# Optimization experiments

Measured on AMD Instinct MI355X. Metric: run time of the kernel, lower is better.

The kernel has to match this reference:

```python
import jax, jax.numpy as jnp
import numpy as np


def _mlp3(x, w0, b0, w1, b1, w2, b2):
    x = jax.nn.relu(x @ w0.T + b0)
    x = jax.nn.relu(x @ w1.T + b1)
    return x @ w2.T + b2


def setup_inputs() -> dict:
    key = jax.random.key(0)
    ks = jax.random.split(key, 32)
    B, T, C, E, H, A = 64, 256, 53, 64, 64, 128
    C2 = C * C
    s = 0.1  # weight scale for numerical stability
    inp = {
        'x': jax.random.normal(ks[0], (B, T, C), jnp.float32),
        'w_emb': s * jax.random.normal(ks[1], (E, 1), jnp.float32),
        'b_emb': s * jax.random.normal(ks[2], (E,), jnp.float32),
        'w_ih': s * jax.random.normal(ks[3], (3 * H, E), jnp.float32),
        'w_hh': s * jax.random.normal(ks[4], (3 * H, H), jnp.float32),
        'b_ih': s * jax.random.normal(ks[5], (3 * H,), jnp.float32),
        'b_hh': s * jax.random.normal(ks[6], (3 * H,), jnp.float32),
        'q_w0': s * jax.random.normal(ks[7], (A, H), jnp.float32),
        'q_b0': s * jax.random.normal(ks[8], (A,), jnp.float32),
        'q_w1': s * jax.random.normal(ks[9], (A, A), jnp.float32),
        'q_b1': s * jax.random.normal(ks[10], (A,), jnp.float32),
        'q_w2': s * jax.random.normal(ks[11], (A, A), jnp.float32),
        'q_b2': s * jax.random.normal(ks[12], (A,), jnp.float32),
        'k_w0': s * jax.random.normal(ks[13], (A, H), jnp.float32),
        'k_b0': s * jax.random.normal(ks[14], (A,), jnp.float32),
        'k_w1': s * jax.random.normal(ks[15], (A, A), jnp.float32),
        'k_b1': s * jax.random.normal(ks[16], (A,), jnp.float32),
        'k_w2': s * jax.random.normal(ks[17], (A, A), jnp.float32),
        'k_b2': s * jax.random.normal(ks[18], (A,), jnp.float32),
        'gate_bias': jax.random.normal(ks[19], (C, C), jnp.float32),
        'pred_w': s * jax.random.normal(ks[20], (1, H), jnp.float32),
        'pred_b': s * jax.random.normal(ks[21], (1,), jnp.float32),
        'clf_w0': 0.02 * jax.random.normal(ks[22], (C2 // 2, C2), jnp.float32),
        'clf_b0': s * jax.random.normal(ks[23], (C2 // 2,), jnp.float32),
        'clf_w1': 0.02 * jax.random.normal(ks[24], (C2 // 4, C2 // 2), jnp.float32),
        'clf_b1': s * jax.random.normal(ks[25], (C2 // 4,), jnp.float32),
        'clf_w2': 0.02 * jax.random.normal(ks[26], (2, C2 // 4), jnp.float32),
        'clf_b2': s * jax.random.normal(ks[27], (2,), jnp.float32),
    }
    return inp


def reference(x, w_emb, b_emb, w_ih, w_hh, b_ih, b_hh,
              q_w0, q_b0, q_w1, q_b1, q_w2, q_b2,
              k_w0, k_b0, k_w1, k_b1, k_w2, k_b2,
              gate_bias, pred_w, pred_b,
              clf_w0, clf_b0, clf_w1, clf_b1, clf_w2, clf_b2):
    B, T, C = x.shape
    H = w_hh.shape[1]
    # single_embed Linear(1, E): embedded[b,t,c,e] = x[b,t,c]*w[e] + b[e]
    embedded = x[..., None] * w_emb[:, 0] + b_emb          # (B,T,C,E)
    emb_t = jnp.transpose(embedded, (1, 0, 2, 3))           # (T,B,C,E)
    h0 = jnp.zeros((B, C, H), x.dtype)

    def step(h, e_t):
        # GRU cell over B*C independent sequences (vectorized as (B,C,*))
        gi = e_t @ w_ih.T + b_ih                            # (B,C,3H)
        gh = h @ w_hh.T + b_hh
        ir, iz, inn = jnp.split(gi, 3, axis=-1)
        hr, hz, hn = jnp.split(gh, 3, axis=-1)
        r = jax.nn.sigmoid(ir + hr)
        z = jax.nn.sigmoid(iz + hz)
        n = jnp.tanh(inn + r * hn)
        h_gru = (1.0 - z) * n + z * h                       # (B,C,H)
        # gated self-attention mixing across components
        q = _mlp3(h_gru, q_w0, q_b0, q_w1, q_b1, q_w2, q_b2)
        k = _mlp3(h_gru, k_w0, k_b0, k_w1, k_b1, k_w2, k_b2)
        transfer = jnp.einsum('bch,bdh->bcd', q, k)         # (B,C,C)
        norms = jnp.sqrt(jnp.sum(transfer * transfer, axis=(1, 2), keepdims=True))
        transfer = transfer / norms                         # Frobenius matrix-norm divide
        gate = jax.nn.sigmoid(jnp.abs(transfer) + gate_bias)
        transfer = transfer * gate
        h_new = jnp.einsum('bcd,bdh->bch', transfer, h_gru)
        return h_new, (h_new, transfer)

    _, (hs, mix) = jax.lax.scan(step, h0, emb_t)
    hs = jnp.transpose(hs, (1, 0, 2, 3))                    # (B,T,C,H)
    mix = jnp.transpose(mix, (1, 0, 2, 3))                  # (B,T,C,C)

    hidden = hs[:, :-1]                                     # (B,T-1,C,H)
    predicted = (hidden @ pred_w.T + pred_b)[..., 0]        # (B,T-1,C)

    clf_in = mix.reshape(B, T, -1)                          # (B,T,C^2)
    mean_FNC = jnp.mean(clf_in, axis=1).reshape(B, C, C)
    z1 = jax.nn.relu(clf_in @ clf_w0.T + clf_b0)            # dropout is identity (eval)
    z2 = jax.nn.relu(z1 @ clf_w1.T + clf_b1)
    logits = jnp.mean(z2 @ clf_w2.T + clf_b2, axis=1)       # (B,2)
    return (logits, mean_FNC, mix, predicted, x[:, 1:, :])
```

## Files before the change

kernel.cpp:

```cpp
#include <hip/hip_runtime.h>
#include <hip/hip_fp16.h>

typedef _Float16 f16;
typedef f16 f16x4 __attribute__((ext_vector_type(4)));
typedef f16 f16x8 __attribute__((ext_vector_type(8)));
typedef float f32x4 __attribute__((ext_vector_type(4)));
typedef float f32x4u __attribute__((ext_vector_type(4), aligned(4)));

#define DEVINL __device__ __forceinline__
#define MFMA16(a, b, c) __builtin_amdgcn_mfma_f32_16x16x32_f16(a, b, c, 0, 0, 0)

DEVINL float sigmoidf_(float v) { return 1.f / (1.f + __expf(-v)); }


__global__ __launch_bounds__(512)
void scan_kernel(const float* __restrict__ x,
                 const float* __restrict__ w_emb,
                 const float* __restrict__ b_emb,
                 const float* __restrict__ w_ih,
                 const float* __restrict__ w_hh,
                 const float* __restrict__ b_ih,
                 const float* __restrict__ b_hh,
                 const float* __restrict__ qw0, const float* __restrict__ qb0,
                 const float* __restrict__ qw1, const float* __restrict__ qb1,
                 const float* __restrict__ qw2, const float* __restrict__ qb2,
                 const float* __restrict__ kw0, const float* __restrict__ kb0,
                 const float* __restrict__ kw1, const float* __restrict__ kb1,
                 const float* __restrict__ kw2, const float* __restrict__ kb2,
                 const float* __restrict__ gate_bias,
                 const float* __restrict__ pred_w,
                 const float* __restrict__ pred_b,
                 float* __restrict__ out_meanF,
                 float* __restrict__ out_mix,
                 float* __restrict__ out_pred,
                 float* __restrict__ out_xcopy)
{
    extern __shared__ __align__(16) unsigned char smem[];
    float* hh  = (float*)smem;
    f16*   hK  = (f16*)(smem + 15232);
    f16*   hC  = (f16*)(smem + 23424);
    f16*   qk0 = (f16*)(smem + 31616);
    f16*   qk1 = (f16*)(smem + 48000);
    f16*   qk2 = (f16*)(smem + 64384);
    f16*   qk3 = (f16*)(smem + 80768);
    f16*   gh  = (f16*)(smem + 31616);
    f16*   trK = (f16*)(smem + 31616);
    float* xc  = (float*)(smem + 97152);
    float* pw  = (float*)(smem + 97376);
    float* red = (float*)(smem + 97632);

    const int b    = blockIdx.x;
    const int tid  = threadIdx.x;
    const int wv   = tid >> 6;
    const int lane = tid & 63;
    const int quad = lane >> 4;
    const int l15  = lane & 15;
    const int colg = (wv << 3) + (lane >> 3);
    const int rsub = lane & 7;

#define FRAG(buf, kt, nt) ((buf) + ((((kt) * 4 + (nt)) * 64 + lane) * 8))

    for (int i = tid; i < 56 * 68; i += 512) hh[i] = 0.f;
    for (int i = tid; i < 4096; i += 512) { hK[i] = (f16)0.f; hC[i] = (f16)0.f; }
    if (tid < 56) xc[tid] = 0.f;
    if (tid < 64) pw[tid] = pred_w[tid];

    float a_r = 0.f, a_z = 0.f, a_n = 0.f, s_r = 0.f, s_z = 0.f, s_n = 0.f;
    for (int e = 0; e < 64; e++) {
        float we = w_emb[e], be = b_emb[e];
        float w0 = w_ih[colg * 64 + e];
        float w1 = w_ih[(64 + colg) * 64 + e];
        float w2 = w_ih[(128 + colg) * 64 + e];
        a_r += w0 * we; s_r += w0 * be;
        a_z += w1 * we; s_z += w1 * be;
        a_n += w2 * we; s_n += w2 * be;
    }
    const float c_r = s_r + b_ih[colg] + b_hh[colg];
    const float c_z = s_z + b_ih[64 + colg] + b_hh[64 + colg];
    const float c_n = s_n + b_ih[128 + colg];
    const float bhn = b_hh[128 + colg];
    const float pb  = pred_b[0];

    auto ldfrag = [&](const float* W, int K, int mt, int kt) -> f16x8 {
        const float* p = W + (size_t)(mt * 16 + l15) * K + kt * 32 + quad * 8;
        float4 u0 = *(const float4*)p;
        float4 u1 = *(const float4*)(p + 4);
        f16x8 a;
        a[0] = (f16)u0.x; a[1] = (f16)u0.y; a[2] = (f16)u0.z; a[3] = (f16)u0.w;
        a[4] = (f16)u1.x; a[5] = (f16)u1.y; a[6] = (f16)u1.z; a[7] = (f16)u1.w;
        return a;
    };

    const int mtLo = (6 * wv) >> 2, mtHi = (6 * wv + 5) >> 2;
    f16x8 wg0k0 = ldfrag(w_hh, 64, mtLo, 0), wg0k1 = ldfrag(w_hh, 64, mtLo, 1);
    f16x8 wg1k0 = ldfrag(w_hh, 64, mtHi, 0), wg1k1 = ldfrag(w_hh, 64, mtHi, 1);

    f16x8 wq0f[2], wk0f[2], wq1f[4], wq2f[4], wk1f[4], wk2f[4];
#pragma unroll
    for (int kt = 0; kt < 2; kt++) {
        wq0f[kt] = ldfrag(qw0, 64, wv, kt);
        wk0f[kt] = ldfrag(kw0, 64, wv, kt);
    }
#pragma unroll
    for (int kt = 0; kt < 4; kt++) {
        wq1f[kt] = ldfrag(qw1, 128, wv, kt);
        wq2f[kt] = ldfrag(qw2, 128, wv, kt);
        wk1f[kt] = ldfrag(kw1, 128, wv, kt);
        wk2f[kt] = ldfrag(kw2, 128, wv, kt);
    }

    const int f0 = wv * 16 + quad * 4;
    f32x4 bq0v, bq1v, bq2v, bk0v, bk1v, bk2v;
#pragma unroll
    for (int r = 0; r < 4; r++) {
        bq0v[r] = qb0[f0 + r]; bq1v[r] = qb1[f0 + r]; bq2v[r] = qb2[f0 + r];
        bk0v[r] = kb0[f0 + r]; bk1v[r] = kb1[f0 + r]; bk2v[r] = kb2[f0 + r];
    }

    const int tmt = wv & 3, tnt0 = (wv >> 2) * 2;
    float gbv[8], mf[8];
#pragma unroll
    for (int i = 0; i < 2; i++)
#pragma unroll
        for (int r = 0; r < 4; r++) {
            int c = tmt * 16 + quad * 4 + r, d = (tnt0 + i) * 16 + l15;
            gbv[i * 4 + r] = (c < 53 && d < 53) ? gate_bias[c * 53 + d] : 0.f;
            mf[i * 4 + r] = 0.f;
        }

    auto cwrite = [&](f16* dst, int ct, const f32x4 acc, const f32x4 bv, bool rel) {
        const int kts  = wv >> 1;
        const int sub  = (2 * wv + (quad >> 1)) & 3;
        const int base = ((kts * 4 + ct) * 64 + (l15 + 16 * sub)) * 8 + (quad & 1) * 4;
        f16x4 p;
#pragma unroll
        for (int r = 0; r < 4; r++) {
            float v = acc[r] + bv[r];
            if (rel) v = fmaxf(v, 0.f);
            p[r] = (f16)v;
        }
        *(f16x4*)(dst + base) = p;
    };

    __syncthreads();

#define MLP4X(WF, SRC, DST, BV, REL) do { \
    f32x4 a0 = {0.f,0.f,0.f,0.f}, a1 = {0.f,0.f,0.f,0.f}; \
    f32x4 a2 = {0.f,0.f,0.f,0.f}, a3 = {0.f,0.f,0.f,0.f}; \
    _Pragma("unroll") for (int kt = 0; kt < 4; kt++) { \
        a0 = MFMA16(WF[kt], *(const f16x8*)FRAG(SRC, kt, 0), a0); \
        a1 = MFMA16(WF[kt], *(const f16x8*)FRAG(SRC, kt, 1), a1); \
        a2 = MFMA16(WF[kt], *(const f16x8*)FRAG(SRC, kt, 2), a2); \
        a3 = MFMA16(WF[kt], *(const f16x8*)FRAG(SRC, kt, 3), a3); } \
    cwrite(DST, 0, a0, BV, REL); cwrite(DST, 1, a1, BV, REL); \
    cwrite(DST, 2, a2, BV, REL); cwrite(DST, 3, a3, BV, REL); } while (0)

    float xv = 0.f;
    if (tid < 53) xv = x[(size_t)b * 256 * 53 + tid];

    for (int t = 0; t < 256; t++) {
        if (tid < 53) xc[tid] = xv;
        {
#pragma unroll
            for (int i = 0; i < 6; i++) {
                int tau = 6 * wv + i, mt = tau >> 2, ct = tau & 3;
                bool hi = (mt != mtLo);
                f32x4 acc = {0.f, 0.f, 0.f, 0.f};
                acc = MFMA16(hi ? wg1k0 : wg0k0, *(const f16x8*)FRAG(hK, 0, ct), acc);
                acc = MFMA16(hi ? wg1k1 : wg0k1, *(const f16x8*)FRAG(hK, 1, ct), acc);
                int gbase = (mt * 16 + quad * 4) * 68 + ct * 16 + l15;
#pragma unroll
                for (int r = 0; r < 4; r++) gh[gbase + r * 68] = (f16)acc[r];
            }
        }
        __syncthreads();
        {
#pragma unroll
            for (int r = 0; r < 7; r++) {
                int c = rsub + 8 * r;
                float hr = (float)gh[colg * 68 + c];
                float hz = (float)gh[(64 + colg) * 68 + c];
                float hn = (float)gh[(128 + colg) * 68 + c];
                float xcv = xc[c];
                float hp = hh[c * 68 + colg];
                float rr = sigmoidf_(xcv * a_r + c_r + hr);
                float zz = sigmoidf_(xcv * a_z + c_z + hz);
                float e2 = __expf(2.f * (xcv * a_n + c_n + rr * (hn + bhn)));
                float nn = 1.f - 2.f / (e2 + 1.f);
                float hg = (1.f - zz) * nn + zz * hp;
                hh[c * 68 + colg] = hg;
                f16 h6 = (f16)hg;
                hK[(((colg >> 5) * 4 + (c >> 4)) * 64 + (c & 15) + 16 * ((colg >> 3) & 3)) * 8 + (colg & 7)] = h6;
                hC[(((c >> 5) * 4 + (colg >> 4)) * 64 + (colg & 15) + 16 * ((c >> 3) & 3)) * 8 + (c & 7)] = h6;
            }
        }
        __syncthreads();
        {
            if (tid < 53) {
                if (t >= 1) out_xcopy[(b * 255 + (t - 1)) * 53 + tid] = xv;
                if (t < 255) xv = x[((size_t)b * 256 + t + 1) * 53 + tid];
            }
            f32x4 a0 = {0.f,0.f,0.f,0.f}, a1 = {0.f,0.f,0.f,0.f};
            f32x4 a2 = {0.f,0.f,0.f,0.f}, a3 = {0.f,0.f,0.f,0.f};
#pragma unroll
            for (int kt = 0; kt < 2; kt++) {
                a0 = MFMA16(wq0f[kt], *(const f16x8*)FRAG(hK, kt, 0), a0);
                a1 = MFMA16(wq0f[kt], *(const f16x8*)FRAG(hK, kt, 1), a1);
                a2 = MFMA16(wq0f[kt], *(const f16x8*)FRAG(hK, kt, 2), a2);
                a3 = MFMA16(wq0f[kt], *(const f16x8*)FRAG(hK, kt, 3), a3);
            }
            cwrite(qk0, 0, a0, bq0v, true); cwrite(qk0, 1, a1, bq0v, true);
            cwrite(qk0, 2, a2, bq0v, true); cwrite(qk0, 3, a3, bq0v, true);
            f32x4 k0 = {0.f,0.f,0.f,0.f}, k1 = {0.f,0.f,0.f,0.f};
            f32x4 k2 = {0.f,0.f,0.f,0.f}, k3 = {0.f,0.f,0.f,0.f};
#pragma unroll
            for (int kt = 0; kt < 2; kt++) {
                k0 = MFMA16(wk0f[kt], *(const f16x8*)FRAG(hK, kt, 0), k0);
                k1 = MFMA16(wk0f[kt], *(const f16x8*)FRAG(hK, kt, 1), k1);
                k2 = MFMA16(wk0f[kt], *(const f16x8*)FRAG(hK, kt, 2), k2);
                k3 = MFMA16(wk0f[kt], *(const f16x8*)FRAG(hK, kt, 3), k3);
            }
            cwrite(qk1, 0, k0, bk0v, true); cwrite(qk1, 1, k1, bk0v, true);
            cwrite(qk1, 2, k2, bk0v, true); cwrite(qk1, 3, k3, bk0v, true);
        }
        __syncthreads();
        MLP4X(wq1f, qk0, qk2, bq1v, true);
        MLP4X(wk1f, qk1, qk3, bk1v, true);
        __syncthreads();
        MLP4X(wq2f, qk2, qk0, bq2v, false);
        MLP4X(wk2f, qk3, qk1, bk2v, false);
        __syncthreads();
        f32x4 tacc0 = {0.f,0.f,0.f,0.f}, tacc1 = {0.f,0.f,0.f,0.f};
        {
            f16x8 qa[4];
#pragma unroll
            for (int kt = 0; kt < 4; kt++) qa[kt] = *(const f16x8*)FRAG(qk0, kt, tmt);
#pragma unroll
            for (int kt = 0; kt < 4; kt++) {
                tacc0 = MFMA16(qa[kt], *(const f16x8*)FRAG(qk1, kt, tnt0), tacc0);
                tacc1 = MFMA16(qa[kt], *(const f16x8*)FRAG(qk1, kt, tnt0 + 1), tacc1);
            }
            float ssq = 0.f;
#pragma unroll
            for (int r = 0; r < 4; r++) {
                int c = tmt * 16 + quad * 4 + r;
                if (c < 53) {
                    if (tnt0 * 16 + l15 < 53)       ssq += tacc0[r] * tacc0[r];
                    if ((tnt0 + 1) * 16 + l15 < 53) ssq += tacc1[r] * tacc1[r];
                }
            }
#pragma unroll
            for (int off = 32; off > 0; off >>= 1) ssq += __shfl_down(ssq, off);
            if (lane == 0) red[wv] = ssq;
        }
        __syncthreads();
        float ov[8];
        {
            float s2 = 0.f;
#pragma unroll
            for (int w8 = 0; w8 < 8; w8++) s2 += red[w8];
            const float inv = rsqrtf(s2);
#pragma unroll
            for (int i = 0; i < 2; i++)
#pragma unroll
                for (int r = 0; r < 4; r++) {
                    int c = tmt * 16 + quad * 4 + r;
                    int d = (tnt0 + i) * 16 + l15;
                    float v = (i == 0 ? tacc0[r] : tacc1[r]) * inv;
                    float g = sigmoidf_(fabsf(v) + gbv[i * 4 + r]);
                    v *= g;
                    bool ok = (c < 53) & (d < 53);
                    v = ok ? v : 0.f;
                    ov[i * 4 + r] = v;
                    mf[i * 4 + r] += v;
                    trK[(((d >> 5) * 4 + (c >> 4)) * 64 + (c & 15) + 16 * ((d >> 3) & 3)) * 8 + (d & 7)] = (f16)v;
                }
        }
        __syncthreads();
        {
            const int mixbase = (b * 256 + t) * 2809;
#pragma unroll
            for (int i = 0; i < 2; i++)
#pragma unroll
                for (int r = 0; r < 4; r++) {
                    int c = tmt * 16 + quad * 4 + r;
                    int d = (tnt0 + i) * 16 + l15;
                    if ((c < 53) & (d < 53)) out_mix[mixbase + c * 53 + d] = ov[i * 4 + r];
                }
        }
        {
            f32x4 h0 = {0.f,0.f,0.f,0.f}, h1 = {0.f,0.f,0.f,0.f};
            f16x8 ta0 = *(const f16x8*)FRAG(trK, 0, tmt);
            f16x8 ta1 = *(const f16x8*)FRAG(trK, 1, tmt);
            h0 = MFMA16(ta0, *(const f16x8*)FRAG(hC, 0, tnt0), h0);
            h0 = MFMA16(ta1, *(const f16x8*)FRAG(hC, 1, tnt0), h0);
            h1 = MFMA16(ta0, *(const f16x8*)FRAG(hC, 0, tnt0 + 1), h1);
            h1 = MFMA16(ta1, *(const f16x8*)FRAG(hC, 1, tnt0 + 1), h1);
#pragma unroll
            for (int i = 0; i < 2; i++)
#pragma unroll
                for (int r = 0; r < 4; r++) {
                    int c = tmt * 16 + quad * 4 + r;
                    int e = (tnt0 + i) * 16 + l15;
                    float v = (i == 0 ? h0[r] : h1[r]);
                    if (c < 56) hh[c * 68 + e] = v;
                    hK[(((e >> 5) * 4 + (c >> 4)) * 64 + (c & 15) + 16 * ((e >> 3) & 3)) * 8 + (e & 7)] = (f16)v;
                }
        }
        __syncthreads();
        if (t < 255 && tid < 53) {
            const float* hrow = hh + tid * 68;
            float s = pb;
#pragma unroll 4
            for (int e4 = 0; e4 < 16; e4++) {
                float4 hv = *(const float4*)(hrow + e4 * 4);
                float4 wv4 = *(const float4*)(pw + e4 * 4);
                s += hv.x * wv4.x + hv.y * wv4.y + hv.z * wv4.z + hv.w * wv4.w;
            }
            out_pred[(b * 255 + t) * 53 + tid] = s;
        }
    }

#pragma unroll
    for (int i = 0; i < 2; i++)
#pragma unroll
        for (int r = 0; r < 4; r++) {
            int c = tmt * 16 + quad * 4 + r;
            int d = (tnt0 + i) * 16 + l15;
            if (c < 53 && d < 53)
                out_meanF[b * 2809 + c * 53 + d] = mf[i * 4 + r] * (1.f / 256.f);
        }
#undef FRAG
#undef MLP4X
}

DEVINL void cvt16(const float* p, f16x8& lo, f16x8& hi) {
    f32x4u u0 = *(const f32x4u*)p;
    f32x4u u1 = *(const f32x4u*)(p + 4);
    f32x4u u2 = *(const f32x4u*)(p + 8);
    f32x4u u3 = *(const f32x4u*)(p + 12);
    lo[0] = (f16)u0.x; lo[1] = (f16)u0.y; lo[2] = (f16)u0.z; lo[3] = (f16)u0.w;
    lo[4] = (f16)u1.x; lo[5] = (f16)u1.y; lo[6] = (f16)u1.z; lo[7] = (f16)u1.w;
    hi[0] = (f16)u2.x; hi[1] = (f16)u2.y; hi[2] = (f16)u2.z; hi[3] = (f16)u2.w;
    hi[4] = (f16)u3.x; hi[5] = (f16)u3.y; hi[6] = (f16)u3.z; hi[7] = (f16)u3.w;
}

template<bool AHALF, bool COLSUM>
__global__ __launch_bounds__(256)
void clf_mfma(const void* __restrict__ Ap,
              const float* __restrict__ W,
              const float* __restrict__ bias,
              __half* __restrict__ z_out,
              float* __restrict__ colsum_out,
              int N, int K, int lda, int Kpad, int ldz)
{
    __shared__ __align__(16) f16 As[4096];
    __shared__ __align__(16) f16 Bs[4096];

    const int tid  = threadIdx.x;
    const int wv   = tid >> 6;
    const int lane = tid & 63;
    const int quad = lane >> 4;
    const int l15  = lane & 15;
    const int wm   = wv & 1;
    const int wn   = wv >> 1;
    const int m0   = blockIdx.x * 128;
    const int n0   = blockIdx.y * 128;

    const int srow = tid >> 1;
    const int skh  = (tid & 1) * 16;
    const int sdst = ((srow >> 4) * 64 + (skh >> 3) * 16 + (srow & 15)) * 8;

    f32x4 acc[4][4];
#pragma unroll
    for (int i = 0; i < 4; i++)
#pragma unroll
        for (int j = 0; j < 4; j++)
            acc[i][j] = (f32x4){0.f, 0.f, 0.f, 0.f};

    for (int k0 = 0; k0 < Kpad; k0 += 32) {
        {
            f16x8 lo, hi;
            if constexpr (AHALF) {
                const f16* p = (const f16*)Ap + (size_t)(m0 + srow) * lda + k0 + skh;
                lo = *(const f16x8*)p;
                hi = *(const f16x8*)(p + 8);
            } else {
                const float* p = (const float*)Ap + (size_t)(m0 + srow) * lda + k0 + skh;
                if (k0 + 32 <= K) {
                    cvt16(p, lo, hi);
                } else {
                    int kr = K - (k0 + skh);
#pragma unroll
                    for (int j = 0; j < 8; j++) lo[j] = (f16)((j < kr) ? p[j] : 0.f);
#pragma unroll
                    for (int j = 0; j < 8; j++) hi[j] = (f16)((j + 8 < kr) ? p[j + 8] : 0.f);
                }
            }
            *(f16x8*)(As + sdst)       = lo;
            *(f16x8*)(As + sdst + 128) = hi;
        }
        {
            f16x8 lo, hi;
#pragma unroll
            for (int j = 0; j < 8; j++) { lo[j] = (f16)0.f; hi[j] = (f16)0.f; }
            const int nrow = n0 + srow;
            if (nrow < N) {
                const float* p = W + (size_t)nrow * K + k0 + skh;
                if (k0 + 32 <= K) {
                    cvt16(p, lo, hi);
                } else {
                    int kr = K - (k0 + skh);
#pragma unroll
                    for (int j = 0; j < 8; j++) lo[j] = (f16)((j < kr) ? p[j] : 0.f);
#pragma unroll
                    for (int j = 0; j < 8; j++) hi[j] = (f16)((j + 8 < kr) ? p[j + 8] : 0.f);
                }
            }
            *(f16x8*)(Bs + sdst)       = lo;
            *(f16x8*)(Bs + sdst + 128) = hi;
        }
        __syncthreads();
        {
            f16x8 afr[4], bfr[4];
#pragma unroll
            for (int i = 0; i < 4; i++)
                afr[i] = *(const f16x8*)(As + ((wm * 4 + i) * 64 + lane) * 8);
#pragma unroll
            for (int i = 0; i < 4; i++)
                bfr[i] = *(const f16x8*)(Bs + ((wn * 4 + i) * 64 + lane) * 8);
#pragma unroll
            for (int mi = 0; mi < 4; mi++)
#pragma unroll
                for (int ni = 0; ni < 4; ni++)
                    acc[mi][ni] = MFMA16(afr[mi], bfr[ni], acc[mi][ni]);
        }
        __syncthreads();
    }

    if constexpr (!COLSUM) {
#pragma unroll
        for (int ni = 0; ni < 4; ni++) {
            int n = n0 + wn * 64 + ni * 16 + l15;
            float bj = (n < N) ? bias[n] : 0.f;
#pragma unroll
            for (int mi = 0; mi < 4; mi++) {
                int m = m0 + wm * 64 + mi * 16 + quad * 4;
#pragma unroll
                for (int r = 0; r < 4; r++) {
                    float v = (n < N) ? fmaxf(acc[mi][ni][r] + bj, 0.f) : 0.f;
                    z_out[(size_t)(m + r) * ldz + n] = __float2half(v);
                }
            }
        }
    } else {
        const int batch = m0 >> 8;
#pragma unroll
        for (int ni = 0; ni < 4; ni++) {
            int n = n0 + wn * 64 + ni * 16 + l15;
            float bj = (n < N) ? bias[n] : 0.f;
            float s = 0.f;
#pragma unroll
            for (int mi = 0; mi < 4; mi++)
#pragma unroll
                for (int r = 0; r < 4; r++)
                    s += fmaxf(acc[mi][ni][r] + bj, 0.f);
            s += __shfl_down(s, 32);
            s += __shfl_down(s, 16);
            if (quad == 0 && n < N)
                atomicAdd(&colsum_out[batch * 704 + n], s);
        }
    }
}

__global__ __launch_bounds__(128)
void logits_kernel(const float* __restrict__ zsum,
                   const float* __restrict__ w2,
                   const float* __restrict__ b2,
                   float* __restrict__ out)
{
    int tid = threadIdx.x;
    int bb = tid >> 1, o = tid & 1;
    const float* zs = zsum + bb * 704;
    const float* wrow = w2 + o * 702;
    float s = 0.f;
    for (int j = 0; j < 702; j++) s += zs[j] * wrow[j];
    out[bb * 2 + o] = s * (1.f / 256.f) + b2[o];
}

extern "C" void kernel_launch(void* const* d_in, const int* in_sizes, int n_in,
                              void* d_out, int out_size, void* d_ws, size_t ws_size,
                              hipStream_t stream)
{
    const float* x      = (const float*)d_in[0];
    const float* w_emb  = (const float*)d_in[1];
    const float* b_emb  = (const float*)d_in[2];
    const float* w_ih   = (const float*)d_in[3];
    const float* w_hh   = (const float*)d_in[4];
    const float* b_ih   = (const float*)d_in[5];
    const float* b_hh   = (const float*)d_in[6];
    const float* qw0 = (const float*)d_in[7];
    const float* qb0 = (const float*)d_in[8];
    const float* qw1 = (const float*)d_in[9];
    const float* qb1 = (const float*)d_in[10];
    const float* qw2 = (const float*)d_in[11];
    const float* qb2 = (const float*)d_in[12];
    const float* kw0 = (const float*)d_in[13];
    const float* kb0 = (const float*)d_in[14];
    const float* kw1 = (const float*)d_in[15];
    const float* kb1 = (const float*)d_in[16];
    const float* kw2 = (const float*)d_in[17];
    const float* kb2 = (const float*)d_in[18];
    const float* gate_bias = (const float*)d_in[19];
    const float* pred_w = (const float*)d_in[20];
    const float* pred_b = (const float*)d_in[21];
    const float* cw0 = (const float*)d_in[22];
    const float* cb0 = (const float*)d_in[23];
    const float* cw1 = (const float*)d_in[24];
    const float* cb1 = (const float*)d_in[25];
    const float* cw2 = (const float*)d_in[26];
    const float* cb2 = (const float*)d_in[27];

    float* out_logits = (float*)d_out;
    float* out_meanF  = (float*)d_out + 128;
    float* out_mix    = (float*)d_out + 128 + 179776;
    float* out_pred   = out_mix + 46022656;
    float* out_xcopy  = out_pred + 864960;

    float*  zsum = (float*)d_ws;
    __half* z1   = (__half*)((char*)d_ws + (1 << 18));

    static int s_attr_done = 0;
    if (!s_attr_done) {
        hipFuncSetAttribute((const void*)scan_kernel,
                            hipFuncAttributeMaxDynamicSharedMemorySize, 98304);
        s_attr_done = 1;
    }

    hipMemsetAsync(zsum, 0, 64 * 704 * sizeof(float), stream);

    scan_kernel<<<64, 512, 97680, stream>>>(
        x, w_emb, b_emb, w_ih, w_hh, b_ih, b_hh,
        qw0, qb0, qw1, qb1, qw2, qb2,
        kw0, kb0, kw1, kb1, kw2, kb2,
        gate_bias, pred_w, pred_b,
        out_meanF, out_mix, out_pred, out_xcopy);

    clf_mfma<false, false><<<dim3(128, 11), 256, 0, stream>>>(
        out_mix, cw0, cb0, z1, nullptr, 1404, 2809, 2809, 2816, 1408);

    clf_mfma<true, true><<<dim3(128, 6), 256, 0, stream>>>(
        z1, cw1, cb1, nullptr, zsum, 702, 1404, 1408, 1408, 0);

    logits_kernel<<<1, 128, 0, stream>>>(zsum, cw2, cb2, out_logits);
}
```

Before: 3.217 ms.

## Process two batch elements per scan block to interleave independent recurrences

The scan kernel now handles two batch sequences per workgroup (32 blocks instead of 64). Each block keeps duplicated shared-memory state for both and interleaves their MFMA stages between the same barriers. The goal is to amortize barrier and latency cost across two independent dependency chains and hide MFMA latency with more ILP. In exchange it uses half the CUs, roughly doubles per-block work, and needs about 162KB of LDS. That exceeds the 64KB documented LDS per workgroup on CDNA3, and MI355X's larger LDS would have to accommodate it. The x load and copy also move from a one-step prefetch to a synchronous load at each step.

New measurement: 7.797 ms. 2.42x slower.

```diff
diff --git a/kernel.cpp b/kernel.cpp
--- a/kernel.cpp
+++ b/kernel.cpp
@@ -36,20 +36,7 @@
                  float* __restrict__ out_xcopy)
 {
     extern __shared__ __align__(16) unsigned char smem[];
-    float* hh  = (float*)smem;
-    f16*   hK  = (f16*)(smem + 15232);
-    f16*   hC  = (f16*)(smem + 23424);
-    f16*   qk0 = (f16*)(smem + 31616);
-    f16*   qk1 = (f16*)(smem + 48000);
-    f16*   qk2 = (f16*)(smem + 64384);
-    f16*   qk3 = (f16*)(smem + 80768);
-    f16*   gh  = (f16*)(smem + 31616);
-    f16*   trK = (f16*)(smem + 31616);
-    float* xc  = (float*)(smem + 97152);
-    float* pw  = (float*)(smem + 97376);
-    float* red = (float*)(smem + 97632);
-
-    const int b    = blockIdx.x;
+
     const int tid  = threadIdx.x;
     const int wv   = tid >> 6;
     const int lane = tid & 63;
@@ -58,11 +45,33 @@
     const int colg = (wv << 3) + (lane >> 3);
     const int rsub = lane & 7;
 
+    float* hh[2]; f16 *hK[2], *hC[2], *qkX[2], *qkY[2], *qkZ[2], *ghp[2], *trKp[2];
+#pragma unroll
+    for (int p = 0; p < 2; p++) {
+        unsigned char* r = smem + p * 80768;
+        hh[p]  = (float*)r;
+        hK[p]  = (f16*)(r + 15232);
+        hC[p]  = (f16*)(r + 23424);
+        qkX[p] = (f16*)(r + 31616);
+        qkY[p] = (f16*)(r + 48000);
+        qkZ[p] = (f16*)(r + 64384);
+        ghp[p] = (f16*)(r + 31616);
+        trKp[p]= (f16*)(r + 31616);
+    }
+    unsigned char* tail = smem + 161536;
+    float* xc[2]  = {(float*)tail, (float*)(tail + 224)};
+    float* pw     = (float*)(tail + 448);
+    float* red[2] = {(float*)(tail + 704), (float*)(tail + 736)};
+
+    const int bb[2] = {(int)blockIdx.x * 2, (int)blockIdx.x * 2 + 1};
+
 #define FRAG(buf, kt, nt) ((buf) + ((((kt) * 4 + (nt)) * 64 + lane) * 8))
 
-    for (int i = tid; i < 56 * 68; i += 512) hh[i] = 0.f;
-    for (int i = tid; i < 4096; i += 512) { hK[i] = (f16)0.f; hC[i] = (f16)0.f; }
-    if (tid < 56) xc[tid] = 0.f;
+#pragma unroll
+    for (int p = 0; p < 2; p++) {
+        for (int i = tid; i < 56 * 68; i += 512) hh[p][i] = 0.f;
+        for (int i = tid; i < 4096; i += 512) { hK[p][i] = (f16)0.f; hC[p][i] = (f16)0.f; }
+    }
     if (tid < 64) pw[tid] = pred_w[tid];
 
     float a_r = 0.f, a_z = 0.f, a_n = 0.f, s_r = 0.f, s_z = 0.f, s_n = 0.f;
@@ -118,184 +127,189 @@
     }
 
     const int tmt = wv & 3, tnt0 = (wv >> 2) * 2;
-    float gbv[8], mf[8];
+    float gbv[8], mf[2][8];
 #pragma unroll
     for (int i = 0; i < 2; i++)
 #pragma unroll
         for (int r = 0; r < 4; r++) {
             int c = tmt * 16 + quad * 4 + r, d = (tnt0 + i) * 16 + l15;
             gbv[i * 4 + r] = (c < 53 && d < 53) ? gate_bias[c * 53 + d] : 0.f;
-            mf[i * 4 + r] = 0.f;
+            mf[0][i * 4 + r] = 0.f; mf[1][i * 4 + r] = 0.f;
         }
 
     auto cwrite = [&](f16* dst, int ct, const f32x4 acc, const f32x4 bv, bool rel) {
         const int kts  = wv >> 1;
         const int sub  = (2 * wv + (quad >> 1)) & 3;
         const int base = ((kts * 4 + ct) * 64 + (l15 + 16 * sub)) * 8 + (quad & 1) * 4;
-        f16x4 p;
+        f16x4 pk;
 #pragma unroll
         for (int r = 0; r < 4; r++) {
             float v = acc[r] + bv[r];
             if (rel) v = fmaxf(v, 0.f);
-            p[r] = (f16)v;
-        }
-        *(f16x4*)(dst + base) = p;
+            pk[r] = (f16)v;
+        }
+        *(f16x4*)(dst + base) = pk;
     };
 
+    auto mlp4 = [&](const f16x8* WF, const f16* SRC, f16* DST, const f32x4 bv, bool rel) {
+        f32x4 a0 = {0.f,0.f,0.f,0.f}, a1 = {0.f,0.f,0.f,0.f};
+        f32x4 a2 = {0.f,0.f,0.f,0.f}, a3 = {0.f,0.f,0.f,0.f};
+#pragma unroll
+        for (int kt = 0; kt < 4; kt++) {
+            a0 = MFMA16(WF[kt], *(const f16x8*)FRAG(SRC, kt, 0), a0);
+            a1 = MFMA16(WF[kt], *(const f16x8*)FRAG(SRC, kt, 1), a1);
+            a2 = MFMA16(WF[kt], *(const f16x8*)FRAG(SRC, kt, 2), a2);
+            a3 = MFMA16(WF[kt], *(const f16x8*)FRAG(SRC, kt, 3), a3);
+        }
+        cwrite(DST, 0, a0, bv, rel); cwrite(DST, 1, a1, bv, rel);
+        cwrite(DST, 2, a2, bv, rel); cwrite(DST, 3, a3, bv, rel);
+    };
+
     __syncthreads();
 
-#define MLP4X(WF, SRC, DST, BV, REL) do { \
-    f32x4 a0 = {0.f,0.f,0.f,0.f}, a1 = {0.f,0.f,0.f,0.f}; \
-    f32x4 a2 = {0.f,0.f,0.f,0.f}, a3 = {0.f,0.f,0.f,0.f}; \
-    _Pragma("unroll") for (int kt = 0; kt < 4; kt++) { \
-        a0 = MFMA16(WF[kt], *(const f16x8*)FRAG(SRC, kt, 0), a0); \
-        a1 = MFMA16(WF[kt], *(const f16x8*)FRAG(SRC, kt, 1), a1); \
-        a2 = MFMA16(WF[kt], *(const f16x8*)FRAG(SRC, kt, 2), a2); \
-        a3 = MFMA16(WF[kt], *(const f16x8*)FRAG(SRC, kt, 3), a3); } \
-    cwrite(DST, 0, a0, BV, REL); cwrite(DST, 1, a1, BV, REL); \
-    cwrite(DST, 2, a2, BV, REL); cwrite(DST, 3, a3, BV, REL); } while (0)
-
-    float xv = 0.f;
-    if (tid < 53) xv = x[(size_t)b * 256 * 53 + tid];
+    f32x4 tacc0[2], tacc1[2];
 
     for (int t = 0; t < 256; t++) {
-        if (tid < 53) xc[tid] = xv;
-        {
+        if (tid < 53) {
+#pragma unroll
+            for (int p = 0; p < 2; p++) {
+                float xv = x[((size_t)bb[p] * 256 + t) * 53 + tid];
+                xc[p][tid] = xv;
+                if (t >= 1) out_xcopy[((size_t)bb[p] * 255 + (t - 1)) * 53 + tid] = xv;
+            }
+        }
+#pragma unroll
+        for (int p = 0; p < 2; p++) {
 #pragma unroll
             for (int i = 0; i < 6; i++) {
                 int tau = 6 * wv + i, mt = tau >> 2, ct = tau & 3;
                 bool hi = (mt != mtLo);
                 f32x4 acc = {0.f, 0.f, 0.f, 0.f};
-                acc = MFMA16(hi ? wg1k0 : wg0k0, *(const f16x8*)FRAG(hK, 0, ct), acc);
-                acc = MFMA16(hi ? wg1k1 : wg0k1, *(const f16x8*)FRAG(hK, 1, ct), acc);
+                acc = MFMA16(hi ? wg1k0 : wg0k0, *(const f16x8*)FRAG(hK[p], 0, ct), acc);
+                acc = MFMA16(hi ? wg1k1 : wg0k1, *(const f16x8*)FRAG(hK[p], 1, ct), acc);
                 int gbase = (mt * 16 + quad * 4) * 68 + ct * 16 + l15;
 #pragma unroll
-                for (int r = 0; r < 4; r++) gh[gbase + r * 68] = (f16)acc[r];
-            }
-        }
-        __syncthreads();
-        {
+                for (int r = 0; r < 4; r++) ghp[p][gbase + r * 68] = (f16)acc[r];
+            }
+        }
+        __syncthreads();
+#pragma unroll
+        for (int p = 0; p < 2; p++) {
 #pragma unroll
             for (int r = 0; r < 7; r++) {
                 int c = rsub + 8 * r;
-                float hr = (float)gh[colg * 68 + c];
-                float hz = (float)gh[(64 + colg) * 68 + c];
-                float hn = (float)gh[(128 + colg) * 68 + c];
-                float xcv = xc[c];
-                float hp = hh[c * 68 + colg];
+                float hr = (float)ghp[p][colg * 68 + c];
+                float hz = (float)ghp[p][(64 + colg) * 68 + c];
+                float hn = (float)ghp[p][(128 + colg) * 68 + c];
+                float xcv = xc[p][c];
+                float hp = hh[p][c * 68 + colg];
                 float rr = sigmoidf_(xcv * a_r + c_r + hr);
                 float zz = sigmoidf_(xcv * a_z + c_z + hz);
                 float e2 = __expf(2.f * (xcv * a_n + c_n + rr * (hn + bhn)));
                 float nn = 1.f - 2.f / (e2 + 1.f);
                 float hg = (1.f - zz) * nn + zz * hp;
-                hh[c * 68 + colg] = hg;
+                hh[p][c * 68 + colg] = hg;
                 f16 h6 = (f16)hg;
-                hK[(((colg >> 5) * 4 + (c >> 4)) * 64 + (c & 15) + 16 * ((colg >> 3) & 3)) * 8 + (colg & 7)] = h6;
-                hC[(((c >> 5) * 4 + (colg >> 4)) * 64 + (colg & 15) + 16 * ((c >> 3) & 3)) * 8 + (c & 7)] = h6;
-            }
-        }
-        __syncthreads();
-        {
-            if (tid < 53) {
-                if (t >= 1) out_xcopy[(b * 255 + (t - 1)) * 53 + tid] = xv;
-                if (t < 255) xv = x[((size_t)b * 256 + t + 1) * 53 + tid];
-            }
+                hK[p][(((colg >> 5) * 4 + (c >> 4)) * 64 + (c & 15) + 16 * ((colg >> 3) & 3)) * 8 + (colg & 7)] = h6;
+                hC[p][(((c >> 5) * 4 + (colg >> 4)) * 64 + (colg & 15) + 16 * ((c >> 3) & 3)) * 8 + (c & 7)] = h6;
+            }
+        }
+        __syncthreads();
+#pragma unroll
+        for (int p = 0; p < 2; p++) {
             f32x4 a0 = {0.f,0.f,0.f,0.f}, a1 = {0.f,0.f,0.f,0.f};
             f32x4 a2 = {0.f,0.f,0.f,0.f}, a3 = {0.f,0.f,0.f,0.f};
 #pragma unroll
             for (int kt = 0; kt < 2; kt++) {
-                a0 = MFMA16(wq0f[kt], *(const f16x8*)FRAG(hK, kt, 0), a0);
-                a1 = MFMA16(wq0f[kt], *(const f16x8*)FRAG(hK, kt, 1), a1);
-                a2 = MFMA16(wq0f[kt], *(const f16x8*)FRAG(hK, kt, 2), a2);
-                a3 = MFMA16(wq0f[kt], *(const f16x8*)FRAG(hK, kt, 3), a3);
-            }
-            cwrite(qk0, 0, a0, bq0v, true); cwrite(qk0, 1, a1, bq0v, true);
-            cwrite(qk0, 2, a2, bq0v, true); cwrite(qk0, 3, a3, bq0v, true);
+                a0 = MFMA16(wq0f[kt], *(const f16x8*)FRAG(hK[p], kt, 0), a0);
+                a1 = MFMA16(wq0f[kt], *(const f16x8*)FRAG(hK[p], kt, 1), a1);
+                a2 = MFMA16(wq0f[kt], *(const f16x8*)FRAG(hK[p], kt, 2), a2);
+                a3 = MFMA16(wq0f[kt], *(const f16x8*)FRAG(hK[p], kt, 3), a3);
+            }
+            cwrite(qkX[p], 0, a0, bq0v, true); cwrite(qkX[p], 1, a1, bq0v, true);
+            cwrite(qkX[p], 2, a2, bq0v, true); cwrite(qkX[p], 3, a3, bq0v, true);
             f32x4 k0 = {0.f,0.f,0.f,0.f}, k1 = {0.f,0.f,0.f,0.f};
             f32x4 k2 = {0.f,0.f,0.f,0.f}, k3 = {0.f,0.f,0.f,0.f};
 #pragma unroll
             for (int kt = 0; kt < 2; kt++) {
-                k0 = MFMA16(wk0f[kt], *(const f16x8*)FRAG(hK, kt, 0), k0);
-                k1 = MFMA16(wk0f[kt], *(const f16x8*)FRAG(hK, kt, 1), k1);
-                k2 = MFMA16(wk0f[kt], *(const f16x8*)FRAG(hK, kt, 2), k2);
-                k3 = MFMA16(wk0f[kt], *(const f16x8*)FRAG(hK, kt, 3), k3);
-            }
-            cwrite(qk1, 0, k0, bk0v, true); cwrite(qk1, 1, k1, bk0v, true);
-            cwrite(qk1, 2, k2, bk0v, true); cwrite(qk1, 3, k3, bk0v, true);
-        }
-        __syncthreads();
-        MLP4X(wq1f, qk0, qk2, bq1v, true);
-        MLP4X(wk1f, qk1, qk3, bk1v, true);
-        __syncthreads();
-        MLP4X(wq2f, qk2, qk0, bq2v, false);
-        MLP4X(wk2f, qk3, qk1, bk2v, false);
-        __syncthreads();
-        f32x4 tacc0 = {0.f,0.f,0.f,0.f}, tacc1 = {0.f,0.f,0.f,0.f};
-        {
-            f16x8 qa[4];
-#pragma unroll
-            for (int kt = 0; kt < 4; kt++) qa[kt] = *(const f16x8*)FRAG(qk0, kt, tmt);
+                k0 = MFMA16(wk0f[kt], *(const f16x8*)FRAG(hK[p], kt, 0), k0);
+                k1 = MFMA16(wk0f[kt], *(const f16x8*)FRAG(hK[p], kt, 1), k1);
+                k2 = MFMA16(wk0f[kt], *(const f16x8*)FRAG(hK[p], kt, 2), k2);
+                k3 = MFMA16(wk0f[kt], *(const f16x8*)FRAG(hK[p], kt, 3), k3);
+            }
+            cwrite(qkY[p], 0, k0, bk0v, true); cwrite(qkY[p], 1, k1, bk0v, true);
+            cwrite(qkY[p], 2, k2, bk0v, true); cwrite(qkY[p], 3, k3, bk0v, true);
+        }
+        __syncthreads();
+#pragma unroll
+        for (int p = 0; p < 2; p++) mlp4(wq1f, qkX[p], qkZ[p], bq1v, true);
+        __syncthreads();
+#pragma unroll
+        for (int p = 0; p < 2; p++) mlp4(wk1f, qkY[p], qkX[p], bk1v, true);
+        __syncthreads();
+#pragma unroll
+        for (int p = 0; p < 2; p++) mlp4(wq2f, qkZ[p], qkY[p], bq2v, false);
+        __syncthreads();
+#pragma unroll
+        for (int p = 0; p < 2; p++) mlp4(wk2f, qkX[p], qkZ[p], bk2v, false);
+        __syncthreads();
+#pragma unroll
+        for (int p = 0; p < 2; p++) {
+            tacc0[p] = (f32x4){0.f,0.f,0.f,0.f};
+            tacc1[p] = (f32x4){0.f,0.f,0.f,0.f};
 #pragma unroll
             for (int kt = 0; kt < 4; kt++) {
-                tacc0 = MFMA16(qa[kt], *(const f16x8*)FRAG(qk1, kt, tnt0), tacc0);
-                tacc1 = MFMA16(qa[kt], *(const f16x8*)FRAG(qk1, kt, tnt0 + 1), tacc1);
+                f16x8 qa = *(const f16x8*)FRAG(qkY[p], kt, tmt);
+                tacc0[p] = MFMA16(qa, *(const f16x8*)FRAG(qkZ[p], kt, tnt0), tacc0[p]);
+                tacc1[p] = MFMA16(qa, *(const f16x8*)FRAG(qkZ[p], kt, tnt0 + 1), tacc1[p]);
             }
             float ssq = 0.f;
 #pragma unroll
             for (int r = 0; r < 4; r++) {
                 int c = tmt * 16 + quad * 4 + r;
                 if (c < 53) {
-                    if (tnt0 * 16 + l15 < 53)       ssq += tacc0[r] * tacc0[r];
-                    if ((tnt0 + 1) * 16 + l15 < 53) ssq += tacc1[r] * tacc1[r];
+                    if (tnt0 * 16 + l15 < 53)       ssq += tacc0[p][r] * tacc0[p][r];
+                    if ((tnt0 + 1) * 16 + l15 < 53) ssq += tacc1[p][r] * tacc1[p][r];
                 }
             }
 #pragma unroll
             for (int off = 32; off > 0; off >>= 1) ssq += __shfl_down(ssq, off);
-            if (lane == 0) red[wv] = ssq;
-        }
-        __syncthreads();
-        float ov[8];
-        {
+            if (lane == 0) red[p][wv] = ssq;
+        }
+        __syncthreads();
+#pragma unroll
+        for (int p = 0; p < 2; p++) {
             float s2 = 0.f;
 #pragma unroll
-            for (int w8 = 0; w8 < 8; w8++) s2 += red[w8];
+            for (int w8 = 0; w8 < 8; w8++) s2 += red[p][w8];
             const float inv = rsqrtf(s2);
+            const size_t mixbase = ((size_t)bb[p] * 256 + t) * 2809;
 #pragma unroll
             for (int i = 0; i < 2; i++)
 #pragma unroll
                 for (int r = 0; r < 4; r++) {
                     int c = tmt * 16 + quad * 4 + r;
                     int d = (tnt0 + i) * 16 + l15;
-                    float v = (i == 0 ? tacc0[r] : tacc1[r]) * inv;
+                    float v = (i == 0 ? tacc0[p][r] : tacc1[p][r]) * inv;
                     float g = sigmoidf_(fabsf(v) + gbv[i * 4 + r]);
                     v *= g;
                     bool ok = (c < 53) & (d < 53);
                     v = ok ? v : 0.f;
-                    ov[i * 4 + r] = v;
-                    mf[i * 4 + r] += v;
-                    trK[(((d >> 5) * 4 + (c >> 4)) * 64 + (c & 15) + 16 * ((d >> 3) & 3)) * 8 + (d & 7)] = (f16)v;
-                }
-        }
-        __syncthreads();
-        {
-            const int mixbase = (b * 256 + t) * 2809;
-#pragma unroll
-            for (int i = 0; i < 2; i++)
-#pragma unroll
-                for (int r = 0; r < 4; r++) {
-                    int c = tmt * 16 + quad * 4 + r;
-                    int d = (tnt0 + i) * 16 + l15;
-                    if ((c < 53) & (d < 53)) out_mix[mixbase + c * 53 + d] = ov[i * 4 + r];
-                }
-        }
-        {
+                    if (ok) out_mix[mixbase + c * 53 + d] = v;
+                    mf[p][i * 4 + r] += v;
+                    trKp[p][(((d >> 5) * 4 + (c >> 4)) * 64 + (c & 15) + 16 * ((d >> 3) & 3)) * 8 + (d & 7)] = (f16)v;
+                }
+        }
+        __syncthreads();
+#pragma unroll
+        for (int p = 0; p < 2; p++) {
             f32x4 h0 = {0.f,0.f,0.f,0.f}, h1 = {0.f,0.f,0.f,0.f};
-            f16x8 ta0 = *(const f16x8*)FRAG(trK, 0, tmt);
-            f16x8 ta1 = *(const f16x8*)FRAG(trK, 1, tmt);
-            h0 = MFMA16(ta0, *(const f16x8*)FRAG(hC, 0, tnt0), h0);
-            h0 = MFMA16(ta1, *(const f16x8*)FRAG(hC, 1, tnt0), h0);
-            h1 = MFMA16(ta0, *(const f16x8*)FRAG(hC, 0, tnt0 + 1), h1);
-            h1 = MFMA16(ta1, *(const f16x8*)FRAG(hC, 1, tnt0 + 1), h1);
+            f16x8 ta0 = *(const f16x8*)FRAG(trKp[p], 0, tmt);
+            f16x8 ta1 = *(const f16x8*)FRAG(trKp[p], 1, tmt);
+            h0 = MFMA16(ta0, *(const f16x8*)FRAG(hC[p], 0, tnt0), h0);
+            h0 = MFMA16(ta1, *(const f16x8*)FRAG(hC[p], 1, tnt0), h0);
+            h1 = MFMA16(ta0, *(const f16x8*)FRAG(hC[p], 0, tnt0 + 1), h1);
+            h1 = MFMA16(ta1, *(const f16x8*)FRAG(hC[p], 1, tnt0 + 1), h1);
 #pragma unroll
             for (int i = 0; i < 2; i++)
 #pragma unroll
@@ -303,35 +317,39 @@
                     int c = tmt * 16 + quad * 4 + r;
                     int e = (tnt0 + i) * 16 + l15;
                     float v = (i == 0 ? h0[r] : h1[r]);
-                    if (c < 56) hh[c * 68 + e] = v;
-                    hK[(((e >> 5) * 4 + (c >> 4)) * 64 + (c & 15) + 16 * ((e >> 3) & 3)) * 8 + (e & 7)] = (f16)v;
+                    if (c < 56) hh[p][c * 68 + e] = v;
+                    hK[p][(((e >> 5) * 4 + (c >> 4)) * 64 + (c & 15) + 16 * ((e >> 3) & 3)) * 8 + (e & 7)] = (f16)v;
                 }
         }
         __syncthreads();
         if (t < 255 && tid < 53) {
-            const float* hrow = hh + tid * 68;
-            float s = pb;
+#pragma unroll
+            for (int p = 0; p < 2; p++) {
+                const float* hrow = hh[p] + tid * 68;
+                float s = pb;
 #pragma unroll 4
-            for (int e4 = 0; e4 < 16; e4++) {
-                float4 hv = *(const float4*)(hrow + e4 * 4);
-                float4 wv4 = *(const float4*)(pw + e4 * 4);
-                s += hv.x * wv4.x + hv.y * wv4.y + hv.z * wv4.z + hv.w * wv4.w;
-            }
-            out_pred[(b * 255 + t) * 53 + tid] = s;
-        }
-    }
-
-#pragma unroll
-    for (int i = 0; i < 2; i++)
-#pragma unroll
-        for (int r = 0; r < 4; r++) {
-            int c = tmt * 16 + quad * 4 + r;
-            int d = (tnt0 + i) * 16 + l15;
-            if (c < 53 && d < 53)
-                out_meanF[b * 2809 + c * 53 + d] = mf[i * 4 + r] * (1.f / 256.f);
-        }
+                for (int e4 = 0; e4 < 16; e4++) {
+                    float4 hv = *(const float4*)(hrow + e4 * 4);
+                    float4 wv4 = *(const float4*)(pw + e4 * 4);
+                    s += hv.x * wv4.x + hv.y * wv4.y + hv.z * wv4.z + hv.w * wv4.w;
+                }
+                out_pred[((size_t)bb[p] * 255 + t) * 53 + tid] = s;
+            }
+        }
+    }
+
+#pragma unroll
+    for (int p = 0; p < 2; p++)
+#pragma unroll
+        for (int i = 0; i < 2; i++)
+#pragma unroll
+            for (int r = 0; r < 4; r++) {
+                int c = tmt * 16 + quad * 4 + r;
+                int d = (tnt0 + i) * 16 + l15;
+                if (c < 53 && d < 53)
+                    out_meanF[(size_t)bb[p] * 2809 + c * 53 + d] = mf[p][i * 4 + r] * (1.f / 256.f);
+            }
 #undef FRAG
-#undef MLP4X
 }
 
 DEVINL void cvt16(const float* p, f16x8& lo, f16x8& hi) {
@@ -530,16 +548,12 @@
     float*  zsum = (float*)d_ws;
     __half* z1   = (__half*)((char*)d_ws + (1 << 18));
 
-    static int s_attr_done = 0;
-    if (!s_attr_done) {
-        hipFuncSetAttribute((const void*)scan_kernel,
-                            hipFuncAttributeMaxDynamicSharedMemorySize, 98304);
-        s_attr_done = 1;
-    }
+    hipFuncSetAttribute((const void*)scan_kernel,
+                        hipFuncAttributeMaxDynamicSharedMemorySize, 162304);
 
     hipMemsetAsync(zsum, 0, 64 * 704 * sizeof(float), stream);
 
-    scan_kernel<<<64, 512, 97680, stream>>>(
+    scan_kernel<<<32, 512, 162304, stream>>>(
         x, w_emb, b_emb, w_ih, w_hh, b_ih, b_hh,
         qw0, qb0, qw1, qb1, qw2, qb2,
         kw0, kb0, kw1, kb1, kw2, kb2,
```

## Split q/k MLP chains across wave halves and reuse register-cached B fragments

Applied to the files above, without the earlier changes.

Waves 0-3 now run the query MLP and waves 4-7 the key MLP, with each wave owning two output row tiles instead of one tile of both chains. For the 128x128 layers, the activation fragments are preloaded into registers once per layer and reused across both row tiles. This roughly halves LDS fragment reads per step in the serial scan loop. In exchange it holds more fragments in VGPRs, so register pressure rises. The change also widens index math to size_t, sets the shared-memory attribute on every call, and trims the dynamic LDS size slightly.

Result: slower. 4.193 ms (+30.3%).

```diff
diff --git a/kernel.cpp b/kernel.cpp
--- a/kernel.cpp
+++ b/kernel.cpp
@@ -41,8 +41,8 @@
     f16*   hC  = (f16*)(smem + 23424);
     f16*   qk0 = (f16*)(smem + 31616);
     f16*   qk1 = (f16*)(smem + 48000);
-    f16*   qk2 = (f16*)(smem + 64384);
-    f16*   qk3 = (f16*)(smem + 80768);
+    f16*   qkZ = (f16*)(smem + 64384);
+    f16*   qkW = (f16*)(smem + 80768);
     f16*   gh  = (f16*)(smem + 31616);
     f16*   trK = (f16*)(smem + 31616);
     float* xc  = (float*)(smem + 97152);
@@ -57,6 +57,9 @@
     const int l15  = lane & 15;
     const int colg = (wv << 3) + (lane >> 3);
     const int rsub = lane & 7;
+
+    const int chain = wv >> 2;
+    const int cw    = wv & 3;
 
 #define FRAG(buf, kt, nt) ((buf) + ((((kt) * 4 + (nt)) * 64 + lane) * 8))
 
@@ -95,27 +98,33 @@
     f16x8 wg0k0 = ldfrag(w_hh, 64, mtLo, 0), wg0k1 = ldfrag(w_hh, 64, mtLo, 1);
     f16x8 wg1k0 = ldfrag(w_hh, 64, mtHi, 0), wg1k1 = ldfrag(w_hh, 64, mtHi, 1);
 
-    f16x8 wq0f[2], wk0f[2], wq1f[4], wq2f[4], wk1f[4], wk2f[4];
-#pragma unroll
-    for (int kt = 0; kt < 2; kt++) {
-        wq0f[kt] = ldfrag(qw0, 64, wv, kt);
-        wk0f[kt] = ldfrag(kw0, 64, wv, kt);
+    const float* Wc0 = chain ? kw0 : qw0;  const float* Bc0 = chain ? kb0 : qb0;
+    const float* Wc1 = chain ? kw1 : qw1;  const float* Bc1 = chain ? kb1 : qb1;
+    const float* Wc2 = chain ? kw2 : qw2;  const float* Bc2 = chain ? kb2 : qb2;
+
+    f16x8 w0f[2][2], w1f[2][4], w2f[2][4];
+    f32x4 b0v[2], b1v[2], b2v[2];
+#pragma unroll
+    for (int t2 = 0; t2 < 2; t2++) {
+        const int mt = cw * 2 + t2;
+#pragma unroll
+        for (int kt = 0; kt < 2; kt++) w0f[t2][kt] = ldfrag(Wc0, 64, mt, kt);
+#pragma unroll
+        for (int kt = 0; kt < 4; kt++) {
+            w1f[t2][kt] = ldfrag(Wc1, 128, mt, kt);
+            w2f[t2][kt] = ldfrag(Wc2, 128, mt, kt);
+        }
+        const int fb = mt * 16 + quad * 4;
+#pragma unroll
+        for (int r = 0; r < 4; r++) {
+            b0v[t2][r] = Bc0[fb + r];
+            b1v[t2][r] = Bc1[fb + r];
+            b2v[t2][r] = Bc2[fb + r];
+        }
     }
-#pragma unroll
-    for (int kt = 0; kt < 4; kt++) {
-        wq1f[kt] = ldfrag(qw1, 128, wv, kt);
-        wq2f[kt] = ldfrag(qw2, 128, wv, kt);
-        wk1f[kt] = ldfrag(kw1, 128, wv, kt);
-        wk2f[kt] = ldfrag(kw2, 128, wv, kt);
-    }
-
-    const int f0 = wv * 16 + quad * 4;
-    f32x4 bq0v, bq1v, bq2v, bk0v, bk1v, bk2v;
-#pragma unroll
-    for (int r = 0; r < 4; r++) {
-        bq0v[r] = qb0[f0 + r]; bq1v[r] = qb1[f0 + r]; bq2v[r] = qb2[f0 + r];
-        bk0v[r] = kb0[f0 + r]; bk1v[r] = kb1[f0 + r]; bk2v[r] = kb2[f0 + r];
-    }
+
+    f16* bufA = chain ? qk1 : qk0;
+    f16* bufM = chain ? qkW : qkZ;
 
     const int tmt = wv & 3, tnt0 = (wv >> 2) * 2;
     float gbv[8], mf[8];
@@ -128,32 +137,41 @@
             mf[i * 4 + r] = 0.f;
         }
 
-    auto cwrite = [&](f16* dst, int ct, const f32x4 acc, const f32x4 bv, bool rel) {
-        const int kts  = wv >> 1;
-        const int sub  = (2 * wv + (quad >> 1)) & 3;
+    auto cwrite = [&](f16* dst, int MT, int ct, const f32x4 acc, const f32x4 bv, bool rel) {
+        const int kts  = MT >> 1;
+        const int sub  = (2 * MT + (quad >> 1)) & 3;
         const int base = ((kts * 4 + ct) * 64 + (l15 + 16 * sub)) * 8 + (quad & 1) * 4;
-        f16x4 p;
+        f16x4 pk;
 #pragma unroll
         for (int r = 0; r < 4; r++) {
             float v = acc[r] + bv[r];
             if (rel) v = fmaxf(v, 0.f);
-            p[r] = (f16)v;
-        }
-        *(f16x4*)(dst + base) = p;
+            pk[r] = (f16)v;
+        }
+        *(f16x4*)(dst + base) = pk;
     };
 
     __syncthreads();
 
-#define MLP4X(WF, SRC, DST, BV, REL) do { \
-    f32x4 a0 = {0.f,0.f,0.f,0.f}, a1 = {0.f,0.f,0.f,0.f}; \
-    f32x4 a2 = {0.f,0.f,0.f,0.f}, a3 = {0.f,0.f,0.f,0.f}; \
-    _Pragma("unroll") for (int kt = 0; kt < 4; kt++) { \
-        a0 = MFMA16(WF[kt], *(const f16x8*)FRAG(SRC, kt, 0), a0); \
-        a1 = MFMA16(WF[kt], *(const f16x8*)FRAG(SRC, kt, 1), a1); \
-        a2 = MFMA16(WF[kt], *(const f16x8*)FRAG(SRC, kt, 2), a2); \
-        a3 = MFMA16(WF[kt], *(const f16x8*)FRAG(SRC, kt, 3), a3); } \
-    cwrite(DST, 0, a0, BV, REL); cwrite(DST, 1, a1, BV, REL); \
-    cwrite(DST, 2, a2, BV, REL); cwrite(DST, 3, a3, BV, REL); } while (0)
+    f16x8 bf[4][4];
+
+#define PRELOAD(SRC) do { \
+    _Pragma("unroll") for (int ct = 0; ct < 4; ct++) \
+        _Pragma("unroll") for (int kt = 0; kt < 4; kt++) \
+            bf[ct][kt] = *(const f16x8*)FRAG(SRC, kt, ct); } while (0)
+
+#define MLP2T(WF, BV, DST, REL) do { \
+    _Pragma("unroll") for (int t2 = 0; t2 < 2; t2++) { \
+        f32x4 a0 = {0.f,0.f,0.f,0.f}, a1 = {0.f,0.f,0.f,0.f}; \
+        f32x4 a2 = {0.f,0.f,0.f,0.f}, a3 = {0.f,0.f,0.f,0.f}; \
+        _Pragma("unroll") for (int kt = 0; kt < 4; kt++) { \
+            a0 = MFMA16(WF[t2][kt], bf[0][kt], a0); \
+            a1 = MFMA16(WF[t2][kt], bf[1][kt], a1); \
+            a2 = MFMA16(WF[t2][kt], bf[2][kt], a2); \
+            a3 = MFMA16(WF[t2][kt], bf[3][kt], a3); } \
+        const int MT = cw * 2 + t2; \
+        cwrite(DST, MT, 0, a0, BV[t2], REL); cwrite(DST, MT, 1, a1, BV[t2], REL); \
+        cwrite(DST, MT, 2, a2, BV[t2], REL); cwrite(DST, MT, 3, a3, BV[t2], REL); } } while (0)
 
     float xv = 0.f;
     if (tid < 53) xv = x[(size_t)b * 256 * 53 + tid];
@@ -197,38 +215,33 @@
         __syncthreads();
         {
             if (tid < 53) {
-                if (t >= 1) out_xcopy[(b * 255 + (t - 1)) * 53 + tid] = xv;
+                if (t >= 1) out_xcopy[((size_t)b * 255 + (t - 1)) * 53 + tid] = xv;
                 if (t < 255) xv = x[((size_t)b * 256 + t + 1) * 53 + tid];
             }
-            f32x4 a0 = {0.f,0.f,0.f,0.f}, a1 = {0.f,0.f,0.f,0.f};
-            f32x4 a2 = {0.f,0.f,0.f,0.f}, a3 = {0.f,0.f,0.f,0.f};
-#pragma unroll
-            for (int kt = 0; kt < 2; kt++) {
-                a0 = MFMA16(wq0f[kt], *(const f16x8*)FRAG(hK, kt, 0), a0);
-                a1 = MFMA16(wq0f[kt], *(const f16x8*)FRAG(hK, kt, 1), a1);
-                a2 = MFMA16(wq0f[kt], *(const f16x8*)FRAG(hK, kt, 2), a2);
-                a3 = MFMA16(wq0f[kt], *(const f16x8*)FRAG(hK, kt, 3), a3);
-            }
-            cwrite(qk0, 0, a0, bq0v, true); cwrite(qk0, 1, a1, bq0v, true);
-            cwrite(qk0, 2, a2, bq0v, true); cwrite(qk0, 3, a3, bq0v, true);
-            f32x4 k0 = {0.f,0.f,0.f,0.f}, k1 = {0.f,0.f,0.f,0.f};
-            f32x4 k2 = {0.f,0.f,0.f,0.f}, k3 = {0.f,0.f,0.f,0.f};
-#pragma unroll
-            for (int kt = 0; kt < 2; kt++) {
-                k0 = MFMA16(wk0f[kt], *(const f16x8*)FRAG(hK, kt, 0), k0);
-                k1 = MFMA16(wk0f[kt], *(const f16x8*)FRAG(hK, kt, 1), k1);
-                k2 = MFMA16(wk0f[kt], *(const f16x8*)FRAG(hK, kt, 2), k2);
-                k3 = MFMA16(wk0f[kt], *(const f16x8*)FRAG(hK, kt, 3), k3);
-            }
-            cwrite(qk1, 0, k0, bk0v, true); cwrite(qk1, 1, k1, bk0v, true);
-            cwrite(qk1, 2, k2, bk0v, true); cwrite(qk1, 3, k3, bk0v, true);
-        }
-        __syncthreads();
-        MLP4X(wq1f, qk0, qk2, bq1v, true);
-        MLP4X(wk1f, qk1, qk3, bk1v, true);
-        __syncthreads();
-        MLP4X(wq2f, qk2, qk0, bq2v, false);
-        MLP4X(wk2f, qk3, qk1, bk2v, false);
+#pragma unroll
+            for (int t2 = 0; t2 < 2; t2++) {
+                f32x4 a0 = {0.f,0.f,0.f,0.f}, a1 = {0.f,0.f,0.f,0.f};
+                f32x4 a2 = {0.f,0.f,0.f,0.f}, a3 = {0.f,0.f,0.f,0.f};
+#pragma unroll
+                for (int kt = 0; kt < 2; kt++) {
+                    a0 = MFMA16(w0f[t2][kt], *(const f16x8*)FRAG(hK, kt, 0), a0);
+                    a1 = MFMA16(w0f[t2][kt], *(const f16x8*)FRAG(hK, kt, 1), a1);
+                    a2 = MFMA16(w0f[t2][kt], *(const f16x8*)FRAG(hK, kt, 2), a2);
+                    a3 = MFMA16(w0f[t2][kt], *(const f16x8*)FRAG(hK, kt, 3), a3);
+                }
+                const int MT = cw * 2 + t2;
+                cwrite(bufA, MT, 0, a0, b0v[t2], true);
+                cwrite(bufA, MT, 1, a1, b0v[t2], true);
+                cwrite(bufA, MT, 2, a2, b0v[t2], true);
+                cwrite(bufA, MT, 3, a3, b0v[t2], true);
+            }
+        }
+        __syncthreads();
+        PRELOAD(bufA);
+        MLP2T(w1f, b1v, bufM, true);
+        __syncthreads();
+        PRELOAD(bufM);
+        MLP2T(w2f, b2v, bufA, false);
         __syncthreads();
         f32x4 tacc0 = {0.f,0.f,0.f,0.f}, tacc1 = {0.f,0.f,0.f,0.f};
         {
@@ -278,7 +291,7 @@
         }
         __syncthreads();
         {
-            const int mixbase = (b * 256 + t) * 2809;
+            const size_t mixbase = ((size_t)b * 256 + t) * 2809;
 #pragma unroll
             for (int i = 0; i < 2; i++)
 #pragma unroll
@@ -317,7 +330,7 @@
                 float4 wv4 = *(const float4*)(pw + e4 * 4);
                 s += hv.x * wv4.x + hv.y * wv4.y + hv.z * wv4.z + hv.w * wv4.w;
             }
-            out_pred[(b * 255 + t) * 53 + tid] = s;
+            out_pred[((size_t)b * 255 + t) * 53 + tid] = s;
         }
     }
 
@@ -328,10 +341,11 @@
             int c = tmt * 16 + quad * 4 + r;
             int d = (tnt0 + i) * 16 + l15;
             if (c < 53 && d < 53)
-                out_meanF[b * 2809 + c * 53 + d] = mf[i * 4 + r] * (1.f / 256.f);
+                out_meanF[(size_t)b * 2809 + c * 53 + d] = mf[i * 4 + r] * (1.f / 256.f);
         }
 #undef FRAG
-#undef MLP4X
+#undef PRELOAD
+#undef MLP2T
 }
 
 DEVINL void cvt16(const float* p, f16x8& lo, f16x8& hi) {
@@ -530,16 +544,12 @@
     float*  zsum = (float*)d_ws;
     __half* z1   = (__half*)((char*)d_ws + (1 << 18));
 
-    static int s_attr_done = 0;
-    if (!s_attr_done) {
-        hipFuncSetAttribute((const void*)scan_kernel,
-                            hipFuncAttributeMaxDynamicSharedMemorySize, 98304);
-        s_attr_done = 1;
-    }
+    hipFuncSetAttribute((const void*)scan_kernel,
+                        hipFuncAttributeMaxDynamicSharedMemorySize, 98304);
 
     hipMemsetAsync(zsum, 0, 64 * 704 * sizeof(float), stream);
 
-    scan_kernel<<<64, 512, 97680, stream>>>(
+    scan_kernel<<<64, 512, 97664, stream>>>(
         x, w_emb, b_emb, w_ih, w_hh, b_ih, b_hh,
         qw0, qb0, qw1, qb1, qw2, qb2,
         kw0, kb0, kw1, kb1, kw2, kb2,
```
